# Kernel optimization log

Measured on AMD Instinct MI355X. Metric: run time of the kernel, lower is better.

Reference implementation:

```python
import jax, jax.numpy as jnp
import numpy as np

# dims: num_time T, batch B, nodes N, feature F(=hidden_dim), heads H(must be 1, see notes)
T, B, N, F, H = 16, 32, 512, 128, 1
E = F * T          # embed_size = hidden_dim * num_time = 2048
D = E // H         # head_dim = 2048


def setup_inputs() -> dict:
    key = jax.random.key(0)
    ks = jax.random.split(key, 9)
    s = 0.02
    return {
        "x":   jax.random.normal(ks[0], (T, B, N, F), dtype=jnp.float32),
        # torch nn.Linear convention: W is [out_features, in_features], y = x @ W.T + b
        "Wq":  jax.random.normal(ks[1], (D, D), dtype=jnp.float32) * s,
        "bq":  jnp.zeros((D,), dtype=jnp.float32),
        "Wk":  jax.random.normal(ks[2], (D, D), dtype=jnp.float32) * s,
        "bk":  jnp.zeros((D,), dtype=jnp.float32),
        "Wv":  jax.random.normal(ks[3], (E, D), dtype=jnp.float32) * s,
        "bv":  jnp.zeros((E,), dtype=jnp.float32),
        "Wfc": jax.random.normal(ks[4], (E, E), dtype=jnp.float32) * s,
        "bfc": jnp.zeros((E,), dtype=jnp.float32),
    }


def reference(x, Wq, bq, Wk, bk, Wv, bv, Wfc, bfc):
    Tt, Bb, Nn, Ff = x.shape
    Ee = Ff * Tt
    # mean over axis 1 of the ORIGINAL [T,B,N,F] tensor (this is the batch axis;
    # the original code calls it node_axis but operates on the un-permuted x)
    x_mean = x.mean(axis=1)                                   # [T, N, F]
    # permute(1,2,3,0).reshape -> [B, N, F*T], then split heads (H=1)
    xr = jnp.transpose(x, (1, 2, 3, 0)).reshape(Bb, Nn, H, Ee // H)
    q = xr @ Wq.T + bq                                        # [B, N, H, D]
    k = xr @ Wk.T + bk                                        # [B, N, H, D]
    v = xr @ Wv.T + bv                                        # [B, N, H, E]
    energy = jnp.einsum('nqhd,nkhd->nhqk', q, k)              # [B, H, N, N]
    attention = jax.nn.softmax(energy / jnp.sqrt(jnp.float32(Ee)), axis=3)
    out = jnp.einsum('nhql,nlhd->nqhd', attention, v).reshape(Bb, Nn, Ee)
    out = out @ Wfc.T + bfc                                   # [B, N, E]
    # faithful to the original's (buggy) view: (nodes, batch, T, F) then permute
    out = jnp.transpose(out.reshape(Nn, Bb, Tt, Ff), (2, 1, 0, 3)).mean(axis=1)  # [T, N, F]
    return x_mean + out, attention
```

## Files before the change

### kernel.cpp

```cpp
#include <hip/hip_runtime.h>

typedef __attribute__((ext_vector_type(8))) __bf16 bf16x8;
typedef __attribute__((ext_vector_type(4))) float floatx4;

__device__ __forceinline__ float bf2f(unsigned short u) {
    union { unsigned int i; float f; } v; v.i = ((unsigned int)u) << 16; return v.f;
}
__device__ __forceinline__ unsigned short f2bf(float f) {
    union { float f; unsigned int i; } v; v.f = f;
    unsigned int u = v.i;
    return (unsigned short)((u + 0x7fffu + ((u >> 16) & 1u)) >> 16);
}

__device__ __forceinline__ void async16(const void* g, void* l) {
    __builtin_amdgcn_global_load_lds(
        (__attribute__((address_space(1))) void*)(g),
        (__attribute__((address_space(3))) void*)(l), 16, 0, 0);
}

__global__ void detect_dtype(const unsigned short* __restrict__ w, int* __restrict__ flag)
{
    int tid = threadIdx.x;
    int cnt = 0;
    for (int i = tid; i < 256; i += 64) {
        unsigned short s = w[2 * i];
        int e = (s >> 7) & 0xFF;
        if (e >= 100 && e <= 126) cnt++;
    }
#pragma unroll
    for (int off = 32; off > 0; off >>= 1) cnt += __shfl_xor(cnt, off);
    if (tid == 0) *flag = (cnt >= 128) ? 1 : 0;
}

__global__ __launch_bounds__(256)
void convert_weights(const void* __restrict__ w5, const void* __restrict__ w7,
                     unsigned short* __restrict__ o5, unsigned short* __restrict__ o7,
                     const int* __restrict__ flag)
{
    const void* in = blockIdx.y ? w7 : w5;
    unsigned short* out = blockIdx.y ? o7 : o5;
    int i = (blockIdx.x * 256 + threadIdx.x) * 4;
    if (*flag) {
        *(uint2*)(out + i) = *(const uint2*)((const unsigned short*)in + i);
    } else {
        float4 f = *(const float4*)((const float*)in + i);
        union { uint2 u; unsigned short s[4]; } W;
        W.s[0] = f2bf(f.x); W.s[1] = f2bf(f.y); W.s[2] = f2bf(f.z); W.s[3] = f2bf(f.w);
        *(uint2*)(out + i) = W.u;
    }
}

__global__ __launch_bounds__(256)
void convert_biases(const void* __restrict__ bq, const void* __restrict__ bv,
                    const void* __restrict__ bfc,
                    unsigned short* __restrict__ bqb, unsigned short* __restrict__ bvb,
                    unsigned short* __restrict__ bfcb, const int* __restrict__ flag)
{
    const int which = blockIdx.x;
    const void* in = which == 0 ? bq : (which == 1 ? bv : bfc);
    unsigned short* out = which == 0 ? bqb : (which == 1 ? bvb : bfcb);
    const float scale = which == 1 ? 32.0f : 1.0f;
    int i = threadIdx.x * 8;
    float f[8];
    if (*flag) {
        const unsigned short* p = (const unsigned short*)in + i;
#pragma unroll
        for (int j = 0; j < 8; j++) f[j] = bf2f(p[j]);
    } else {
        float4 a = *(const float4*)((const float*)in + i);
        float4 b = *(const float4*)((const float*)in + i + 4);
        f[0] = a.x; f[1] = a.y; f[2] = a.z; f[3] = a.w;
        f[4] = b.x; f[5] = b.y; f[6] = b.z; f[7] = b.w;
    }
    union { uint4 u; unsigned short s[8]; } W;
#pragma unroll
    for (int j = 0; j < 8; j++) W.s[j] = f2bf(f[j] * scale);
    *(uint4*)(out + i) = W.u;
}

__global__ __launch_bounds__(256)
void transpose_conv(const void* __restrict__ in, unsigned short* __restrict__ out,
                    const int* __restrict__ flag)
{
    __shared__ unsigned short tile[64 * 65];
    const int d0 = blockIdx.x * 64, i0 = blockIdx.y * 64;
    const int tid = threadIdx.x;
    const int r = tid >> 2, seg = tid & 3;

    const long base = (long)(d0 + r) * 2048 + i0 + seg * 16;
    unsigned short vals[16];
    if (*flag) {
        const unsigned short* p = (const unsigned short*)in + base;
        union { uint4 u; unsigned short s[8]; } a, b;
        a.u = *(const uint4*)p; b.u = *(const uint4*)(p + 8);
#pragma unroll
        for (int j = 0; j < 8; j++) { vals[j] = a.s[j]; vals[8 + j] = b.s[j]; }
    } else {
        const float* p = (const float*)in + base;
#pragma unroll
        for (int q = 0; q < 4; q++) {
            float4 v = *(const float4*)(p + q * 4);
            vals[q * 4 + 0] = f2bf(v.x); vals[q * 4 + 1] = f2bf(v.y);
            vals[q * 4 + 2] = f2bf(v.z); vals[q * 4 + 3] = f2bf(v.w);
        }
    }
#pragma unroll
    for (int j = 0; j < 16; j++) tile[r * 65 + seg * 16 + j] = vals[j];
    __syncthreads();

    union { uint4 u[2]; unsigned short s[16]; } W;
#pragma unroll
    for (int j = 0; j < 16; j++) W.s[j] = tile[(seg * 16 + j) * 65 + r];
    unsigned short* o = out + (long)(i0 + r) * 2048 + d0 + seg * 16;
    *(uint4*)o = W.u[0];
    *(uint4*)(o + 8) = W.u[1];
}

__global__ __launch_bounds__(256)
void build_xr(const void* __restrict__ xv, unsigned short* __restrict__ xr,
              const int* __restrict__ flag)
{
    __shared__ __align__(16) unsigned short tile[128 * 24];
    const int bn = blockIdx.x;
    const int b = bn >> 9, n = bn & 511;
    const int tid = threadIdx.x;
    const int t = tid >> 4, l16 = tid & 15;

    const long off = (long)(t * 32 + b) * 65536 + n * 128 + l16 * 8;
    union { uint4 u; unsigned short s[8]; } U;
    if (*flag) {
        U.u = *(const uint4*)((const unsigned short*)xv + off);
    } else {
        const float* xf = (const float*)xv + off;
        float4 f0 = *(const float4*)xf;
        float4 f1 = *(const float4*)(xf + 4);
        U.s[0] = f2bf(f0.x); U.s[1] = f2bf(f0.y); U.s[2] = f2bf(f0.z); U.s[3] = f2bf(f0.w);
        U.s[4] = f2bf(f1.x); U.s[5] = f2bf(f1.y); U.s[6] = f2bf(f1.z); U.s[7] = f2bf(f1.w);
    }
#pragma unroll
    for (int j = 0; j < 8; j++) tile[(l16 * 8 + j) * 24 + t] = U.s[j];
    __syncthreads();

    const int f = tid >> 1, t0 = (tid & 1) * 8;
    uint4 o = *(const uint4*)&tile[f * 24 + t0];
    *(uint4*)(xr + (long)bn * 2048 + tid * 8) = o;
}

template <int MODE, bool BIAS, bool BDIRECT>
__global__ __launch_bounds__(256)
void gemm_nt(const unsigned short* __restrict__ Ag,
             const unsigned short* __restrict__ Bg,
             void* __restrict__ Cg,
             const unsigned short* __restrict__ bias,
             int K, long sA, long sB, long sC, int lda, int ldb, int ldc)
{
    __shared__ __align__(16) unsigned short lsA[128 * 32];
    __shared__ __align__(16) unsigned short lsB[BDIRECT ? 8 : 128 * 32];

    const int tid = threadIdx.x;
    const int z = blockIdx.z;
    const unsigned short* A = Ag + (long)z * sA + (long)blockIdx.y * 128 * lda;
    const unsigned short* B = Bg + (long)z * sB + (long)blockIdx.x * 128 * ldb;

    const int wave = tid >> 6, lane = tid & 63;
    const int wm = (wave >> 1) * 64, wn = (wave & 1) * 64;
    const int r = lane & 15, quad = lane >> 4;

    floatx4 acc[4][4];
#pragma unroll
    for (int i = 0; i < 4; i++)
#pragma unroll
        for (int j = 0; j < 4; j++) acc[i][j] = floatx4{0.f, 0.f, 0.f, 0.f};

    const int srow = tid >> 2;
    const int scol = (tid & 3) * 8;
    const long a0 = (long)srow * lda + scol;
    const long a1 = (long)(srow + 64) * lda + scol;
    const long b0 = (long)srow * ldb + scol;
    const long b1 = (long)(srow + 64) * ldb + scol;

    for (int k0 = 0; k0 < K; k0 += 32) {
        async16(A + k0 + a0, (char*)lsA + tid * 16);
        async16(A + k0 + a1, (char*)lsA + 4096 + tid * 16);
        bf16x8 bb[4];
        if (BDIRECT) {
#pragma unroll
            for (int j = 0; j < 4; j++)
                bb[j] = *(const bf16x8*)(B + (long)(wn + j * 16 + r) * ldb + k0 + quad * 8);
        } else {
            async16(B + k0 + b0, (char*)lsB + tid * 16);
            async16(B + k0 + b1, (char*)lsB + 4096 + tid * 16);
        }
        __syncthreads();

        const bf16x8* pA = (const bf16x8*)lsA;
        bf16x8 af[4];
#pragma unroll
        for (int i = 0; i < 4; i++) af[i] = pA[(wm + i * 16 + r) * 4 + quad];
        if (!BDIRECT) {
            const bf16x8* pB = (const bf16x8*)lsB;
#pragma unroll
            for (int j = 0; j < 4; j++) bb[j] = pB[(wn + j * 16 + r) * 4 + quad];
        }
#pragma unroll
        for (int i = 0; i < 4; i++)
#pragma unroll
            for (int j = 0; j < 4; j++)
                acc[i][j] = __builtin_amdgcn_mfma_f32_16x16x32_bf16(af[i], bb[j], acc[i][j], 0, 0, 0);
        __syncthreads();
    }

    const int mb = blockIdx.y * 128 + wm + quad * 4;
    const int nb = blockIdx.x * 128 + wn + r;

    if (MODE == 1) {
        float* C = (float*)Cg + (long)z * sC;
#pragma unroll
        for (int i = 0; i < 4; i++)
#pragma unroll
            for (int j = 0; j < 4; j++)
#pragma unroll
                for (int g = 0; g < 4; g++)
                    C[(long)(mb + i * 16 + g) * ldc + (nb + j * 16)] = acc[i][j][g];
    } else {
        unsigned short* C = (unsigned short*)Cg + (long)z * sC;
#pragma unroll
        for (int j = 0; j < 4; j++) {
            const int n = nb + j * 16;
            const float bj = BIAS ? bf2f(bias[n]) : 0.0f;
#pragma unroll
            for (int i = 0; i < 4; i++)
#pragma unroll
                for (int g = 0; g < 4; g++)
                    C[(long)(mb + i * 16 + g) * ldc + n] = f2bf(acc[i][j][g] + bj);
        }
    }
}

__global__ __launch_bounds__(256)
void w2_kernel(const unsigned short* __restrict__ WkT,
               const unsigned short* __restrict__ bqb, float* __restrict__ w2)
{
    const int i = blockIdx.x, tid = threadIdx.x;
    const unsigned short* row = WkT + (long)i * 2048 + tid * 8;
    const unsigned short* bv = bqb + tid * 8;
    union { uint4 u; unsigned short s[8]; } A, B;
    A.u = *(const uint4*)row; B.u = *(const uint4*)bv;
    float s = 0.f;
#pragma unroll
    for (int j = 0; j < 8; j++) s += bf2f(A.s[j]) * bf2f(B.s[j]);
#pragma unroll
    for (int off = 32; off > 0; off >>= 1) s += __shfl_xor(s, off);
    __shared__ float red[4];
    if ((tid & 63) == 0) red[tid >> 6] = s;
    __syncthreads();
    if (tid == 0) w2[i] = red[0] + red[1] + red[2] + red[3];
}

__global__ __launch_bounds__(256)
void c_kernel(const unsigned short* __restrict__ xr, const float* __restrict__ w2,
              float* __restrict__ c)
{
    const int row = blockIdx.x * 4 + (threadIdx.x >> 6);
    const int lane = threadIdx.x & 63;
    float s = 0.f;
#pragma unroll
    for (int ch = 0; ch < 4; ch++) {
        const int i0 = ch * 512 + lane * 8;
        union { uint4 u; unsigned short s[8]; } X;
        X.u = *(const uint4*)(xr + (long)row * 2048 + i0);
        float4 w0 = *(const float4*)(w2 + i0);
        float4 w1 = *(const float4*)(w2 + i0 + 4);
        s += bf2f(X.s[0]) * w0.x + bf2f(X.s[1]) * w0.y + bf2f(X.s[2]) * w0.z + bf2f(X.s[3]) * w0.w;
        s += bf2f(X.s[4]) * w1.x + bf2f(X.s[5]) * w1.y + bf2f(X.s[6]) * w1.z + bf2f(X.s[7]) * w1.w;
    }
#pragma unroll
    for (int off = 32; off > 0; off >>= 1) s += __shfl_xor(s, off);
    if (lane == 0) c[row] = s;
}

__global__ __launch_bounds__(256)
void softmax_pbar(const float* __restrict__ S, const float* __restrict__ c,
                  void* __restrict__ dout, unsigned short* __restrict__ Pbar,
                  const int* __restrict__ flag)
{
    const int g = blockIdx.x;
    const int b = g >> 4;
    const int tid = threadIdx.x;
    const float scale = 0.02209708691207961f;
    const int isbf = *flag;
    __shared__ float redm[4], reds[4];

    float2 cv = ((const float2*)(c + b * 512))[tid];
    float p0 = 0.f, p1 = 0.f;

    for (int r = 0; r < 32; r++) {
        const long row = (long)g * 32 + r;
        float2 v = ((const float2*)(S + row * 512))[tid];
        float a = (v.x + cv.x) * scale, d = (v.y + cv.y) * scale;

        float m = fmaxf(a, d);
#pragma unroll
        for (int off = 32; off > 0; off >>= 1) m = fmaxf(m, __shfl_xor(m, off));
        if ((tid & 63) == 0) redm[tid >> 6] = m;
        __syncthreads();
        m = fmaxf(fmaxf(redm[0], redm[1]), fmaxf(redm[2], redm[3]));

        float ea = __expf(a - m), eb = __expf(d - m);
        float s = ea + eb;
#pragma unroll
        for (int off = 32; off > 0; off >>= 1) s += __shfl_xor(s, off);
        if ((tid & 63) == 0) reds[tid >> 6] = s;
        __syncthreads();
        s = reds[0] + reds[1] + reds[2] + reds[3];
        const float inv = 1.0f / s;
        const float fa = ea * inv, fb = eb * inv;
        p0 += fa; p1 += fb;

        if (isbf) {
            unsigned short* P = (unsigned short*)dout + 1048576;
            ((unsigned int*)(P + row * 512))[tid] =
                (unsigned int)f2bf(fa) | ((unsigned int)f2bf(fb) << 16);
        } else {
            float* P = (float*)dout + 1048576;
            ((float2*)(P + row * 512))[tid] = make_float2(fa, fb);
        }
        __syncthreads();
    }
    ((unsigned int*)(Pbar + (long)g * 512))[tid] =
        (unsigned int)f2bf(p0) | ((unsigned int)f2bf(p1) << 16);
}

__global__ __launch_bounds__(256)
void z_kernel(const unsigned short* __restrict__ Pbar,
              const unsigned short* __restrict__ xr,
              unsigned short* __restrict__ Z)
{
    __shared__ __align__(16) unsigned short tile[32 * 64];
    const int b = blockIdx.y, d0 = blockIdx.x * 64;
    const int tid = threadIdx.x;
    const int wave = tid >> 6, lane = tid & 63;
    const int r = lane & 15, quad = lane >> 4;
    const unsigned short* xrb = xr + (long)b * 512 * 2048;

    floatx4 acc = floatx4{0.f, 0.f, 0.f, 0.f};
    for (int l0 = 0; l0 < 512; l0 += 32) {
        async16(xrb + (long)(l0 + (tid >> 3)) * 2048 + d0 + (tid & 7) * 8,
                (char*)tile + tid * 16);
        __syncthreads();
        bf16x8 a = *(const bf16x8*)(Pbar + (long)(b * 16 + r) * 512 + l0 + quad * 8);
        union { bf16x8 v; unsigned short s[8]; } bb;
#pragma unroll
        for (int j = 0; j < 8; j++) bb.s[j] = tile[(quad * 8 + j) * 64 + wave * 16 + r];
        acc = __builtin_amdgcn_mfma_f32_16x16x32_bf16(a, bb.v, acc, 0, 0, 0);
        __syncthreads();
    }
#pragma unroll
    for (int g = 0; g < 4; g++)
        Z[(long)(b * 16 + quad * 4 + g) * 2048 + d0 + wave * 16 + r] = f2bf(acc[g]);
}

__global__ __launch_bounds__(256)
void final_small(const unsigned short* __restrict__ xr,
                 const unsigned short* __restrict__ Ybar,
                 const unsigned short* __restrict__ bfcb, void* __restrict__ dout,
                 const int* __restrict__ flag)
{
    __shared__ float xm[2048];
    const int n = blockIdx.x;
    const int tid = threadIdx.x;
    const int isbf = *flag;

    float a[8] = {0, 0, 0, 0, 0, 0, 0, 0};
    const unsigned short* base = xr + (long)n * 2048 + tid * 8;
    for (int b = 0; b < 32; b++) {
        union { uint4 u; unsigned short s[8]; } U;
        U.u = *(const uint4*)(base + (long)b * 1048576);
#pragma unroll
        for (int j = 0; j < 8; j++) a[j] += bf2f(U.s[j]);
    }
#pragma unroll
    for (int j = 0; j < 8; j++) xm[tid * 8 + j] = a[j];
    __syncthreads();

    const int col0 = tid * 8;
    const int t = col0 >> 7, f0 = col0 & 127;
    float acc[8];
    {
        union { uint4 u; unsigned short s[8]; } Yv, Bv;
        Yv.u = *(const uint4*)(Ybar + (long)n * 2048 + col0);
        Bv.u = *(const uint4*)(bfcb + col0);
#pragma unroll
        for (int j = 0; j < 8; j++)
            acc[j] = bf2f(Yv.s[j]) + 32.0f * bf2f(Bv.s[j]) + xm[(f0 + j) * 16 + t];
    }
    const long oidx = (long)t * 65536 + n * 128 + f0;
    if (isbf) {
        union { uint4 u; unsigned short s[8]; } W;
#pragma unroll
        for (int j = 0; j < 8; j++) W.s[j] = f2bf(acc[j] * 0.03125f);
        *(uint4*)((unsigned short*)dout + oidx) = W.u;
    } else {
        float* o = (float*)dout + oidx;
#pragma unroll
        for (int j = 0; j < 8; j += 4)
            *(float4*)(o + j) = make_float4(acc[j] * 0.03125f, acc[j + 1] * 0.03125f,
                                            acc[j + 2] * 0.03125f, acc[j + 3] * 0.03125f);
    }
}

extern "C" void kernel_launch(void* const* d_in, const int* in_sizes, int n_in,
                              void* d_out, int out_size, void* d_ws, size_t ws_size,
                              hipStream_t stream)
{
    unsigned short* xr   = (unsigned short*)d_ws;
    unsigned short* H    = xr + 33554432;
    float*          S    = (float*)(H + 33554432);
    unsigned short* Gt   = (unsigned short*)(S + 8388608);
    unsigned short* WqT  = Gt  + 4194304;
    unsigned short* WkT  = WqT + 4194304;
    unsigned short* Wvb  = WkT + 4194304;
    unsigned short* Wfcb = Wvb + 4194304;
    unsigned short* Pbar = Wfcb + 4194304;
    unsigned short* Z    = Pbar + 262144;
    unsigned short* Obar = Z + 1048576;
    unsigned short* Ybar = Obar + 1048576;
    unsigned short* bqb  = Ybar + 1048576;
    unsigned short* bvb  = bqb + 2048;
    unsigned short* bfcb = bvb + 2048;
    float*          w2   = (float*)(bfcb + 2048);
    float*          c    = w2 + 2048;
    int*            flag = (int*)(c + 16384);

    detect_dtype<<<1, 64, 0, stream>>>((const unsigned short*)d_in[1], flag);
    transpose_conv<<<dim3(32, 32), 256, 0, stream>>>(d_in[1], WqT, flag);
    transpose_conv<<<dim3(32, 32), 256, 0, stream>>>(d_in[3], WkT, flag);
    convert_weights<<<dim3(4096, 2), 256, 0, stream>>>(d_in[5], d_in[7], Wvb, Wfcb, flag);
    convert_biases<<<3, 256, 0, stream>>>(d_in[2], d_in[6], d_in[8], bqb, bvb, bfcb, flag);

    build_xr<<<16384, 256, 0, stream>>>(d_in[0], xr, flag);
    gemm_nt<0, false, true><<<dim3(16, 16, 1), 256, 0, stream>>>(
        WkT, WqT, Gt, nullptr, 2048, 0, 0, 0, 2048, 2048, 2048);
    gemm_nt<0, false, true><<<dim3(16, 128, 1), 256, 0, stream>>>(
        xr, Gt, H, nullptr, 2048, 0, 0, 0, 2048, 2048, 2048);
    w2_kernel<<<2048, 256, 0, stream>>>(WkT, bqb, w2);
    c_kernel<<<4096, 256, 0, stream>>>(xr, w2, c);
    gemm_nt<1, false, false><<<dim3(4, 4, 32), 256, 0, stream>>>(
        H, xr, S, nullptr, 2048, 1048576, 1048576, 262144, 2048, 2048, 512);
    softmax_pbar<<<512, 256, 0, stream>>>(S, c, d_out, Pbar, flag);
    z_kernel<<<dim3(32, 32), 256, 0, stream>>>(Pbar, xr, Z);
    gemm_nt<0, true, true><<<dim3(16, 4, 1), 256, 0, stream>>>(
        Z, Wvb, Obar, bvb, 2048, 0, 0, 0, 2048, 2048, 2048);
    gemm_nt<0, false, true><<<dim3(16, 4, 1), 256, 0, stream>>>(
        Obar, Wfcb, Ybar, nullptr, 2048, 0, 0, 0, 2048, 2048, 2048);
    final_small<<<512, 256, 0, stream>>>(xr, Ybar, bfcb, d_out, flag);
}
```

Baseline: 931.8 us.

## Fuse row-bias dot into build_xr, drop BDIRECT, add 64-row GEMM tiles

Computes the per-row c = xr·w2 inside build_xr, with a block reduction, and removes the separate c_kernel pass over xr. w2_kernel now runs before build_xr so the fused kernel has its input. The GEMM template drops the direct-from-global B path and always stages B through LDS. It also adds a BM=64 variant with four waves along N, used for the small-M GEMMs to launch more blocks. The tradeoff is an extra reduction and scattered w2 reads in build_xr, and fewer MFMAs per wave in the 64-row tiles.

Result: faster. 751.5 us (-19.4%).

```diff
diff --git a/kernel.cpp b/kernel.cpp
--- a/kernel.cpp
+++ b/kernel.cpp
@@ -118,9 +118,11 @@
 
 __global__ __launch_bounds__(256)
 void build_xr(const void* __restrict__ xv, unsigned short* __restrict__ xr,
+              const float* __restrict__ w2, float* __restrict__ c,
               const int* __restrict__ flag)
 {
     __shared__ __align__(16) unsigned short tile[128 * 24];
+    __shared__ float red[4];
     const int bn = blockIdx.x;
     const int b = bn >> 9, n = bn & 511;
     const int tid = threadIdx.x;
@@ -137,16 +139,24 @@
         U.s[0] = f2bf(f0.x); U.s[1] = f2bf(f0.y); U.s[2] = f2bf(f0.z); U.s[3] = f2bf(f0.w);
         U.s[4] = f2bf(f1.x); U.s[5] = f2bf(f1.y); U.s[6] = f2bf(f1.z); U.s[7] = f2bf(f1.w);
     }
-#pragma unroll
-    for (int j = 0; j < 8; j++) tile[(l16 * 8 + j) * 24 + t] = U.s[j];
+    float s = 0.f;
+#pragma unroll
+    for (int j = 0; j < 8; j++) {
+        tile[(l16 * 8 + j) * 24 + t] = U.s[j];
+        s += bf2f(U.s[j]) * w2[(l16 * 8 + j) * 16 + t];
+    }
+#pragma unroll
+    for (int o = 32; o > 0; o >>= 1) s += __shfl_xor(s, o);
+    if ((tid & 63) == 0) red[tid >> 6] = s;
     __syncthreads();
+    if (tid == 0) c[bn] = red[0] + red[1] + red[2] + red[3];
 
     const int f = tid >> 1, t0 = (tid & 1) * 8;
     uint4 o = *(const uint4*)&tile[f * 24 + t0];
     *(uint4*)(xr + (long)bn * 2048 + tid * 8) = o;
 }
 
-template <int MODE, bool BIAS, bool BDIRECT>
+template <int MODE, bool BIAS, int BM>
 __global__ __launch_bounds__(256)
 void gemm_nt(const unsigned short* __restrict__ Ag,
              const unsigned short* __restrict__ Bg,
@@ -154,23 +164,25 @@
              const unsigned short* __restrict__ bias,
              int K, long sA, long sB, long sC, int lda, int ldb, int ldc)
 {
-    __shared__ __align__(16) unsigned short lsA[128 * 32];
-    __shared__ __align__(16) unsigned short lsB[BDIRECT ? 8 : 128 * 32];
+    constexpr int NJ = (BM == 128) ? 4 : 2;
+    __shared__ __align__(16) unsigned short lsA[BM * 32];
+    __shared__ __align__(16) unsigned short lsB[128 * 32];
 
     const int tid = threadIdx.x;
     const int z = blockIdx.z;
-    const unsigned short* A = Ag + (long)z * sA + (long)blockIdx.y * 128 * lda;
+    const unsigned short* A = Ag + (long)z * sA + (long)blockIdx.y * BM * lda;
     const unsigned short* B = Bg + (long)z * sB + (long)blockIdx.x * 128 * ldb;
 
     const int wave = tid >> 6, lane = tid & 63;
-    const int wm = (wave >> 1) * 64, wn = (wave & 1) * 64;
+    const int wm = (BM == 128) ? (wave >> 1) * 64 : 0;
+    const int wn = (BM == 128) ? (wave & 1) * 64 : wave * 32;
     const int r = lane & 15, quad = lane >> 4;
 
-    floatx4 acc[4][4];
+    floatx4 acc[4][NJ];
 #pragma unroll
     for (int i = 0; i < 4; i++)
 #pragma unroll
-        for (int j = 0; j < 4; j++) acc[i][j] = floatx4{0.f, 0.f, 0.f, 0.f};
+        for (int j = 0; j < NJ; j++) acc[i][j] = floatx4{0.f, 0.f, 0.f, 0.f};
 
     const int srow = tid >> 2;
     const int scol = (tid & 3) * 8;
@@ -181,36 +193,27 @@
 
     for (int k0 = 0; k0 < K; k0 += 32) {
         async16(A + k0 + a0, (char*)lsA + tid * 16);
-        async16(A + k0 + a1, (char*)lsA + 4096 + tid * 16);
-        bf16x8 bb[4];
-        if (BDIRECT) {
-#pragma unroll
-            for (int j = 0; j < 4; j++)
-                bb[j] = *(const bf16x8*)(B + (long)(wn + j * 16 + r) * ldb + k0 + quad * 8);
-        } else {
-            async16(B + k0 + b0, (char*)lsB + tid * 16);
-            async16(B + k0 + b1, (char*)lsB + 4096 + tid * 16);
-        }
+        if (BM == 128) async16(A + k0 + a1, (char*)lsA + 4096 + tid * 16);
+        async16(B + k0 + b0, (char*)lsB + tid * 16);
+        async16(B + k0 + b1, (char*)lsB + 4096 + tid * 16);
         __syncthreads();
 
         const bf16x8* pA = (const bf16x8*)lsA;
-        bf16x8 af[4];
+        const bf16x8* pB = (const bf16x8*)lsB;
+        bf16x8 af[4], bb[NJ];
 #pragma unroll
         for (int i = 0; i < 4; i++) af[i] = pA[(wm + i * 16 + r) * 4 + quad];
-        if (!BDIRECT) {
-            const bf16x8* pB = (const bf16x8*)lsB;
-#pragma unroll
-            for (int j = 0; j < 4; j++) bb[j] = pB[(wn + j * 16 + r) * 4 + quad];
-        }
+#pragma unroll
+        for (int j = 0; j < NJ; j++) bb[j] = pB[(wn + j * 16 + r) * 4 + quad];
 #pragma unroll
         for (int i = 0; i < 4; i++)
 #pragma unroll
-            for (int j = 0; j < 4; j++)
+            for (int j = 0; j < NJ; j++)
                 acc[i][j] = __builtin_amdgcn_mfma_f32_16x16x32_bf16(af[i], bb[j], acc[i][j], 0, 0, 0);
         __syncthreads();
     }
 
-    const int mb = blockIdx.y * 128 + wm + quad * 4;
+    const int mb = blockIdx.y * BM + wm + quad * 4;
     const int nb = blockIdx.x * 128 + wn + r;
 
     if (MODE == 1) {
@@ -218,14 +221,14 @@
 #pragma unroll
         for (int i = 0; i < 4; i++)
 #pragma unroll
-            for (int j = 0; j < 4; j++)
+            for (int j = 0; j < NJ; j++)
 #pragma unroll
                 for (int g = 0; g < 4; g++)
                     C[(long)(mb + i * 16 + g) * ldc + (nb + j * 16)] = acc[i][j][g];
     } else {
         unsigned short* C = (unsigned short*)Cg + (long)z * sC;
 #pragma unroll
-        for (int j = 0; j < 4; j++) {
+        for (int j = 0; j < NJ; j++) {
             const int n = nb + j * 16;
             const float bj = BIAS ? bf2f(bias[n]) : 0.0f;
 #pragma unroll
@@ -255,28 +258,6 @@
     if ((tid & 63) == 0) red[tid >> 6] = s;
     __syncthreads();
     if (tid == 0) w2[i] = red[0] + red[1] + red[2] + red[3];
-}
-
-__global__ __launch_bounds__(256)
-void c_kernel(const unsigned short* __restrict__ xr, const float* __restrict__ w2,
-              float* __restrict__ c)
-{
-    const int row = blockIdx.x * 4 + (threadIdx.x >> 6);
-    const int lane = threadIdx.x & 63;
-    float s = 0.f;
-#pragma unroll
-    for (int ch = 0; ch < 4; ch++) {
-        const int i0 = ch * 512 + lane * 8;
-        union { uint4 u; unsigned short s[8]; } X;
-        X.u = *(const uint4*)(xr + (long)row * 2048 + i0);
-        float4 w0 = *(const float4*)(w2 + i0);
-        float4 w1 = *(const float4*)(w2 + i0 + 4);
-        s += bf2f(X.s[0]) * w0.x + bf2f(X.s[1]) * w0.y + bf2f(X.s[2]) * w0.z + bf2f(X.s[3]) * w0.w;
-        s += bf2f(X.s[4]) * w1.x + bf2f(X.s[5]) * w1.y + bf2f(X.s[6]) * w1.z + bf2f(X.s[7]) * w1.w;
-    }
-#pragma unroll
-    for (int off = 32; off > 0; off >>= 1) s += __shfl_xor(s, off);
-    if (lane == 0) c[row] = s;
 }
 
 __global__ __launch_bounds__(256)
@@ -437,21 +418,20 @@
     transpose_conv<<<dim3(32, 32), 256, 0, stream>>>(d_in[3], WkT, flag);
     convert_weights<<<dim3(4096, 2), 256, 0, stream>>>(d_in[5], d_in[7], Wvb, Wfcb, flag);
     convert_biases<<<3, 256, 0, stream>>>(d_in[2], d_in[6], d_in[8], bqb, bvb, bfcb, flag);
-
-    build_xr<<<16384, 256, 0, stream>>>(d_in[0], xr, flag);
-    gemm_nt<0, false, true><<<dim3(16, 16, 1), 256, 0, stream>>>(
+    w2_kernel<<<2048, 256, 0, stream>>>(WkT, bqb, w2);
+
+    build_xr<<<16384, 256, 0, stream>>>(d_in[0], xr, w2, c, flag);
+    gemm_nt<0, false, 64><<<dim3(16, 32, 1), 256, 0, stream>>>(
         WkT, WqT, Gt, nullptr, 2048, 0, 0, 0, 2048, 2048, 2048);
-    gemm_nt<0, false, true><<<dim3(16, 128, 1), 256, 0, stream>>>(
+    gemm_nt<0, false, 128><<<dim3(16, 128, 1), 256, 0, stream>>>(
         xr, Gt, H, nullptr, 2048, 0, 0, 0, 2048, 2048, 2048);
-    w2_kernel<<<2048, 256, 0, stream>>>(WkT, bqb, w2);
-    c_kernel<<<4096, 256, 0, stream>>>(xr, w2, c);
-    gemm_nt<1, false, false><<<dim3(4, 4, 32), 256, 0, stream>>>(
+    gemm_nt<1, false, 128><<<dim3(4, 4, 32), 256, 0, stream>>>(
         H, xr, S, nullptr, 2048, 1048576, 1048576, 262144, 2048, 2048, 512);
     softmax_pbar<<<512, 256, 0, stream>>>(S, c, d_out, Pbar, flag);
     z_kernel<<<dim3(32, 32), 256, 0, stream>>>(Pbar, xr, Z);
-    gemm_nt<0, true, true><<<dim3(16, 4, 1), 256, 0, stream>>>(
+    gemm_nt<0, true, 64><<<dim3(16, 8, 1), 256, 0, stream>>>(
         Z, Wvb, Obar, bvb, 2048, 0, 0, 0, 2048, 2048, 2048);
-    gemm_nt<0, false, true><<<dim3(16, 4, 1), 256, 0, stream>>>(
+    gemm_nt<0, false, 64><<<dim3(16, 8, 1), 256, 0, stream>>>(
         Obar, Wfcb, Ybar, nullptr, 2048, 0, 0, 0, 2048, 2048, 2048);
     final_small<<<512, 256, 0, stream>>>(xr, Ybar, bfcb, d_out, flag);
 }
```
